# Kernel tuning notes

Measured on AMD Instinct MI355X. Metric: run time of the kernel, lower is better.

## Reference

```python
import jax, jax.numpy as jnp
import numpy as np

WH, WW = 8, 8
NUM_HEADS = 12
DIM = 384
N = WH * WW

def _rel_pos_index():
    # Swin relative position index, static [N, N] int array
    coords = np.stack(np.meshgrid(np.arange(WH), np.arange(WW), indexing='ij'))  # [2, wh, ww]
    cf = coords.reshape(2, -1)                      # [2, N]
    rel = cf[:, :, None] - cf[:, None, :]           # [2, N, N]
    rel = rel.transpose(1, 2, 0).copy()             # [N, N, 2]
    rel[..., 0] += WH - 1
    rel[..., 1] += WW - 1
    rel[..., 0] *= 2 * WW - 1
    return jnp.asarray(rel.sum(-1))                 # [N, N]

REL_IDX = _rel_pos_index()


def setup_inputs() -> dict:
    key = jax.random.key(0)
    ks = jax.random.split(key, 4)
    Bn = 4096
    x = jax.random.normal(ks[0], (Bn, N, DIM), dtype=jnp.float32)
    qkv_w = jax.random.normal(ks[1], (3 * DIM, DIM), dtype=jnp.float32) * 0.02
    qkv_b = jnp.zeros((3 * DIM,), dtype=jnp.float32)
    proj_w = jax.random.normal(ks[2], (DIM, DIM), dtype=jnp.float32) * 0.02
    proj_b = jnp.zeros((DIM,), dtype=jnp.float32)
    bias_table = jax.random.normal(ks[3], ((2 * WH - 1) * (2 * WW - 1), NUM_HEADS), dtype=jnp.float32) * 0.02
    return {"x": x, "qkv_w": qkv_w, "qkv_b": qkv_b, "proj_w": proj_w, "proj_b": proj_b, "bias_table": bias_table}


def reference(x, qkv_w, qkv_b, proj_w, proj_b, bias_table):
    Bn, n, C = x.shape
    H = NUM_HEADS
    hd = C // H
    scale = hd ** (-0.5)
    qkv = (x @ qkv_w.T + qkv_b).reshape(Bn, n, 3, H, hd)
    q = qkv[:, :, 0].transpose(0, 2, 1, 3)  # [Bn, H, n, hd]
    k = qkv[:, :, 1].transpose(0, 2, 1, 3)
    v = qkv[:, :, 2].transpose(0, 2, 1, 3)
    attn = jnp.einsum('bhqd,bhkd->bhqk', q, k) * scale  # [Bn, H, n, n]
    bias = bias_table[REL_IDX]                           # [n, n, H]
    attn = attn + bias.transpose(2, 0, 1)[None]          # add rel-pos bias
    attn = jax.nn.softmax(attn, axis=-1)
    out = jnp.einsum('bhqk,bhkd->bqhd', attn, v).reshape(Bn, n, C)
    return out @ proj_w.T + proj_b
```

## Files before the change

### kernel.cpp

```cpp
#include <hip/hip_runtime.h>

#define NT 64
#define NH 12
#define HD 32
#define DIM 384
#define NWIN 4096
#define TPB 512
#define PTPB 256

typedef __bf16 bf16;
typedef __bf16 bf16x8 __attribute__((ext_vector_type(8)));
typedef __bf16 bf16x4 __attribute__((ext_vector_type(4)));
typedef float floatx4 __attribute__((ext_vector_type(4)));

__device__ __align__(16) bf16 g_wqkv[3 * DIM * DIM];
__device__ __align__(16) bf16 g_wproj[DIM * DIM];
__device__ __align__(16) float g_biasT[NH * 225];

__global__ void convert_weights(const float* __restrict__ qkv_w,
                                const float* __restrict__ proj_w,
                                const float* __restrict__ bias_table) {
    int i = blockIdx.x * blockDim.x + threadIdx.x;
    if (i < 3 * DIM * DIM) g_wqkv[i] = (bf16)qkv_w[i];
    if (i < DIM * DIM)     g_wproj[i] = (bf16)proj_w[i];
    if (i < NH * 225) {
        int h = i / 225, ix = i % 225;
        g_biasT[i] = bias_table[ix * NH + h];
    }
}

__global__ __launch_bounds__(TPB, 4) void attn_kernel(
    const float* __restrict__ x,
    const float* __restrict__ qkv_b,
    float* __restrict__ out)
{
    __shared__ __align__(16) char smem[65288];
    bf16 (*sx)[392]      = (bf16(*)[392])smem;
    bf16 (*sq2)[64][40]  = (bf16(*)[64][40])smem;
    bf16 (*sk2)[64][40]  = (bf16(*)[64][40])(smem + 10240);
    bf16 (*svT2)[32][72] = (bf16(*)[32][72])(smem + 20480);
    float (*sp2)[64][66] = (float(*)[64][66])(smem + 29696);
    float (*sbias)[225]  = (float(*)[225])(smem + 63488);

    const int t    = threadIdx.x;
    const int win  = blockIdx.x;
    const int wave = t >> 6;
    const int lane = t & 63;
    const int quad = lane >> 4;
    const int l15  = lane & 15;

    {
        const float4* src = (const float4*)(x + (size_t)win * (NT * DIM));
        #pragma unroll
        for (int it = 0; it < (NT * DIM / 4) / TPB; ++it) {
            int i = t + it * TPB;
            float4 fv = src[i];
            int r = i / (DIM / 4);
            int c = (i % (DIM / 4)) * 4;
            bf16x4 bv;
            bv[0] = (bf16)fv.x; bv[1] = (bf16)fv.y;
            bv[2] = (bf16)fv.z; bv[3] = (bf16)fv.w;
            *(bf16x4*)&sx[r][c] = bv;
        }
    }
    __syncthreads();

    const int mt  = wave & 3;
    const int grp = wave >> 2;
    bf16x8 afrag[DIM / 32];
    #pragma unroll
    for (int ks = 0; ks < DIM / 32; ++ks)
        afrag[ks] = *(const bf16x8*)&sx[mt * 16 + l15][ks * 32 + quad * 8];
    __syncthreads();

    const float scale = 0.17677669529663687f;
    float* outw = out + (size_t)win * (NT * DIM);

    #pragma unroll 1
    for (int hp = 0; hp < NH / 2; ++hp) {
        if (t < 225)                      sbias[0][t]       = g_biasT[(hp * 2 + 0) * 225 + t];
        else if (t >= 256 && t < 481)     sbias[1][t - 256] = g_biasT[(hp * 2 + 1) * 225 + (t - 256)];

        #pragma unroll
        for (int jj = 0; jj < 6; ++jj) {
            const int hl  = jj / 3;
            const int j3  = jj % 3;
            const int nt  = grp * 3 + j3;
            const int s   = nt >> 1;
            const int nhh = (nt & 1) * 16;
            const int h   = hp * 2 + hl;
            const int wrow = s * DIM + h * HD + nhh + l15;
            const bf16* Wp = g_wqkv + (size_t)wrow * DIM + quad * 8;
            bf16x8 b[12];
            #pragma unroll
            for (int ks = 0; ks < 12; ++ks) b[ks] = *(const bf16x8*)(Wp + ks * 32);
            floatx4 acc = {0.f, 0.f, 0.f, 0.f};
            #pragma unroll
            for (int ks = 0; ks < 12; ++ks)
                acc = __builtin_amdgcn_mfma_f32_16x16x32_bf16(afrag[ks], b[ks], acc, 0, 0, 0);
            float bv = qkv_b[wrow];
            #pragma unroll
            for (int r = 0; r < 4; ++r) {
                int m = mt * 16 + quad * 4 + r;
                float v = acc[r] + bv;
                if (s == 0)      sq2[hl][m][nhh + l15] = (bf16)(v * scale);
                else if (s == 1) sk2[hl][m][nhh + l15] = (bf16)v;
                else             svT2[hl][nhh + l15][m] = (bf16)v;
            }
        }
        __syncthreads();

        #pragma unroll
        for (int jj = 0; jj < 4; ++jj) {
            int job = wave + jj * 8;
            int hl = job >> 4;
            int j4 = job & 15;
            int it = j4 & 3, jt = j4 >> 2;
            bf16x8 a = *(const bf16x8*)&sq2[hl][it * 16 + l15][quad * 8];
            bf16x8 b = *(const bf16x8*)&sk2[hl][jt * 16 + l15][quad * 8];
            floatx4 acc = {0.f, 0.f, 0.f, 0.f};
            acc = __builtin_amdgcn_mfma_f32_16x16x32_bf16(a, b, acc, 0, 0, 0);
            #pragma unroll
            for (int r = 0; r < 4; ++r) {
                int i = it * 16 + quad * 4 + r;
                int j = jt * 16 + l15;
                int yi = i >> 3, xi = i & 7, yj = j >> 3, xj = j & 7;
                int idx = (yi - yj + 7) * 15 + (xi - xj + 7);
                sp2[hl][i][j] = acc[r] + sbias[hl][idx];
            }
        }
        __syncthreads();

        {
            int r4 = t >> 2;
            int hl = r4 >> 6;
            int r  = r4 & 63;
            int o  = (t & 3) * 16;
            const float2* pr = (const float2*)&sp2[hl][r][0];
            float e[16];
            float mx = -1e30f;
            #pragma unroll
            for (int c = 0; c < 8; ++c) {
                float2 f2 = pr[(o >> 1) + c];
                e[2 * c] = f2.x; e[2 * c + 1] = f2.y;
                mx = fmaxf(mx, fmaxf(f2.x, f2.y));
            }
            mx = fmaxf(mx, __shfl_xor(mx, 1));
            mx = fmaxf(mx, __shfl_xor(mx, 2));
            float sum = 0.f;
            #pragma unroll
            for (int c = 0; c < 16; ++c) { e[c] = __expf(e[c] - mx); sum += e[c]; }
            sum += __shfl_xor(sum, 1);
            sum += __shfl_xor(sum, 2);
            float inv = 1.0f / sum;
            bf16* pw = (bf16*)&sp2[hl][r][0];
            #pragma unroll
            for (int k = 0; k < 4; ++k) {
                bf16x4 pv;
                #pragma unroll
                for (int z = 0; z < 4; ++z) pv[z] = (bf16)(e[4 * k + z] * inv);
                *(bf16x4*)&pw[o + 4 * k] = pv;
            }
        }
        __syncthreads();

        #pragma unroll
        for (int jj = 0; jj < 2; ++jj) {
            int job = wave + jj * 8;
            int hl = job >> 3;
            int j3 = job & 7;
            int pmt = j3 & 3, pnt = j3 >> 2;
            const bf16* prow = (const bf16*)&sp2[hl][pmt * 16 + l15][0];
            floatx4 acc = {0.f, 0.f, 0.f, 0.f};
            #pragma unroll
            for (int ks = 0; ks < 2; ++ks) {
                bf16x4 a0 = *(const bf16x4*)&prow[ks * 32 + quad * 8];
                bf16x4 a1 = *(const bf16x4*)&prow[ks * 32 + quad * 8 + 4];
                bf16x8 av;
                #pragma unroll
                for (int z = 0; z < 4; ++z) { av[z] = a0[z]; av[z + 4] = a1[z]; }
                bf16x8 b = *(const bf16x8*)&svT2[hl][pnt * 16 + l15][ks * 32 + quad * 8];
                acc = __builtin_amdgcn_mfma_f32_16x16x32_bf16(av, b, acc, 0, 0, 0);
            }
            int h = hp * 2 + hl;
            #pragma unroll
            for (int r = 0; r < 4; ++r) {
                int m = pmt * 16 + quad * 4 + r;
                outw[(size_t)m * DIM + h * HD + pnt * 16 + l15] = acc[r];
            }
        }
        __syncthreads();
    }
}

__global__ __launch_bounds__(PTPB, 3) void proj_kernel(
    const float* __restrict__ proj_b,
    float* __restrict__ out)
{
    __shared__ __align__(16) bf16 sa[NT][392];
    const int t    = threadIdx.x;
    const int wave = t >> 6;
    const int lane = t & 63;
    const int quad = lane >> 4;
    const int l15  = lane & 15;
    float* base = out + (size_t)blockIdx.x * (NT * DIM);

    {
        const float4* src = (const float4*)base;
        #pragma unroll
        for (int it = 0; it < (NT * DIM / 4) / PTPB; ++it) {
            int i = t + it * PTPB;
            float4 fv = src[i];
            int r = i / (DIM / 4);
            int c = (i % (DIM / 4)) * 4;
            bf16x4 bv;
            bv[0] = (bf16)fv.x; bv[1] = (bf16)fv.y;
            bv[2] = (bf16)fv.z; bv[3] = (bf16)fv.w;
            *(bf16x4*)&sa[r][c] = bv;
        }
    }
    __syncthreads();

    bf16x8 afrag[DIM / 32];
    #pragma unroll
    for (int ks = 0; ks < DIM / 32; ++ks)
        afrag[ks] = *(const bf16x8*)&sa[wave * 16 + l15][ks * 32 + quad * 8];

    #pragma unroll
    for (int nt = 0; nt < DIM / 16; ++nt) {
        const bf16* Wp = g_wproj + (size_t)(nt * 16 + l15) * DIM + quad * 8;
        bf16x8 b[12];
        #pragma unroll
        for (int ks = 0; ks < 12; ++ks) b[ks] = *(const bf16x8*)(Wp + ks * 32);
        floatx4 acc = {0.f, 0.f, 0.f, 0.f};
        #pragma unroll
        for (int ks = 0; ks < 12; ++ks)
            acc = __builtin_amdgcn_mfma_f32_16x16x32_bf16(afrag[ks], b[ks], acc, 0, 0, 0);
        float pb = proj_b[nt * 16 + l15];
        #pragma unroll
        for (int r = 0; r < 4; ++r)
            base[(size_t)(wave * 16 + quad * 4 + r) * DIM + nt * 16 + l15] = acc[r] + pb;
    }
}

extern "C" void kernel_launch(void* const* d_in, const int* in_sizes, int n_in,
                              void* d_out, int out_size, void* d_ws, size_t ws_size,
                              hipStream_t stream) {
    const float* x          = (const float*)d_in[0];
    const float* qkv_w      = (const float*)d_in[1];
    const float* qkv_b      = (const float*)d_in[2];
    const float* proj_w     = (const float*)d_in[3];
    const float* proj_b     = (const float*)d_in[4];
    const float* bias_table = (const float*)d_in[5];
    float* out = (float*)d_out;

    convert_weights<<<dim3((3 * DIM * DIM + 255) / 256), dim3(256), 0, stream>>>(qkv_w, proj_w, bias_table);
    attn_kernel<<<dim3(NWIN), dim3(TPB), 0, stream>>>(x, qkv_b, out);
    proj_kernel<<<dim3(NWIN), dim3(PTPB), 0, stream>>>(proj_b, out);
}
```

Baseline: 2.654 ms.

## Fuse scores, softmax and PV per wave in registers with double-buffered QKV

Each wave now computes the QK^T scores for its own 16 rows and one head, adds the relative-position bias, applies softmax with cross-lane shuffles in registers, and runs the PV matmul. This removes the fp32 score buffer in shared memory and three of the four block barriers per head pair. Q, K and V are double-buffered across head pairs, V^T and P use XOR-swizzled layouts, and the bias is precomputed into a full [H,64,64] table read from global memory. The x and attention-output staging through shared memory is replaced by direct per-lane float loads converted to bf16, and the GEMM accumulators are split into two chains. The costs are a larger shared-memory footprint, more global bias traffic, and uncoalesced direct global loads.

```diff
diff --git a/kernel.cpp b/kernel.cpp
--- a/kernel.cpp
+++ b/kernel.cpp
@@ -10,12 +10,11 @@
 
 typedef __bf16 bf16;
 typedef __bf16 bf16x8 __attribute__((ext_vector_type(8)));
-typedef __bf16 bf16x4 __attribute__((ext_vector_type(4)));
 typedef float floatx4 __attribute__((ext_vector_type(4)));
 
 __device__ __align__(16) bf16 g_wqkv[3 * DIM * DIM];
 __device__ __align__(16) bf16 g_wproj[DIM * DIM];
-__device__ __align__(16) float g_biasT[NH * 225];
+__device__ __align__(16) float g_biasF[NH * NT * NT];
 
 __global__ void convert_weights(const float* __restrict__ qkv_w,
                                 const float* __restrict__ proj_w,
@@ -23,10 +22,21 @@
     int i = blockIdx.x * blockDim.x + threadIdx.x;
     if (i < 3 * DIM * DIM) g_wqkv[i] = (bf16)qkv_w[i];
     if (i < DIM * DIM)     g_wproj[i] = (bf16)proj_w[i];
-    if (i < NH * 225) {
-        int h = i / 225, ix = i % 225;
-        g_biasT[i] = bias_table[ix * NH + h];
+    if (i < NH * NT * NT) {
+        int h = i >> 12, qk = i & 4095;
+        int q = qk >> 6, kv = qk & 63;
+        int idx = ((q >> 3) - (kv >> 3) + 7) * 15 + ((q & 7) - (kv & 7) + 7);
+        g_biasF[i] = bias_table[idx * NH + h];
     }
+}
+
+__device__ inline bf16x8 load_cvt8(const float* p) {
+    float4 f0 = *(const float4*)p;
+    float4 f1 = *(const float4*)(p + 4);
+    bf16x8 a;
+    a[0] = (bf16)f0.x; a[1] = (bf16)f0.y; a[2] = (bf16)f0.z; a[3] = (bf16)f0.w;
+    a[4] = (bf16)f1.x; a[5] = (bf16)f1.y; a[6] = (bf16)f1.z; a[7] = (bf16)f1.w;
+    return a;
 }
 
 __global__ __launch_bounds__(TPB, 4) void attn_kernel(
@@ -34,13 +44,11 @@
     const float* __restrict__ qkv_b,
     float* __restrict__ out)
 {
-    __shared__ __align__(16) char smem[65288];
-    bf16 (*sx)[392]      = (bf16(*)[392])smem;
-    bf16 (*sq2)[64][40]  = (bf16(*)[64][40])smem;
-    bf16 (*sk2)[64][40]  = (bf16(*)[64][40])(smem + 10240);
-    bf16 (*svT2)[32][72] = (bf16(*)[32][72])(smem + 20480);
-    float (*sp2)[64][66] = (float(*)[64][66])(smem + 29696);
-    float (*sbias)[225]  = (float(*)[225])(smem + 63488);
+    __shared__ __align__(16) char smem[73728];
+    bf16 (*sq)[2][64][40] = (bf16(*)[2][64][40])smem;
+    bf16 (*sk)[2][64][40] = (bf16(*)[2][64][40])(smem + 20480);
+    bf16* svT = (bf16*)(smem + 40960);
+    bf16* sP  = (bf16*)(smem + 57344);
 
     const int t    = threadIdx.x;
     const int win  = blockIdx.x;
@@ -48,156 +56,139 @@
     const int lane = t & 63;
     const int quad = lane >> 4;
     const int l15  = lane & 15;
-
-    {
-        const float4* src = (const float4*)(x + (size_t)win * (NT * DIM));
-        #pragma unroll
-        for (int it = 0; it < (NT * DIM / 4) / TPB; ++it) {
-            int i = t + it * TPB;
-            float4 fv = src[i];
-            int r = i / (DIM / 4);
-            int c = (i % (DIM / 4)) * 4;
-            bf16x4 bv;
-            bv[0] = (bf16)fv.x; bv[1] = (bf16)fv.y;
-            bv[2] = (bf16)fv.z; bv[3] = (bf16)fv.w;
-            *(bf16x4*)&sx[r][c] = bv;
-        }
-    }
-    __syncthreads();
-
-    const int mt  = wave & 3;
-    const int grp = wave >> 2;
-    bf16x8 afrag[DIM / 32];
+    const int mt   = wave & 3;
+    const int grp  = wave >> 2;
+
+    const float* xw = x + (size_t)win * (NT * DIM);
+    bf16x8 afrag[12];
     #pragma unroll
-    for (int ks = 0; ks < DIM / 32; ++ks)
-        afrag[ks] = *(const bf16x8*)&sx[mt * 16 + l15][ks * 32 + quad * 8];
-    __syncthreads();
+    for (int ks = 0; ks < 12; ++ks)
+        afrag[ks] = load_cvt8(xw + (mt * 16 + l15) * DIM + ks * 32 + quad * 8);
 
     const float scale = 0.17677669529663687f;
     float* outw = out + (size_t)win * (NT * DIM);
+    bf16* const sPw = sP + wave * 1024;
 
     #pragma unroll 1
     for (int hp = 0; hp < NH / 2; ++hp) {
-        if (t < 225)                      sbias[0][t]       = g_biasT[(hp * 2 + 0) * 225 + t];
-        else if (t >= 256 && t < 481)     sbias[1][t - 256] = g_biasT[(hp * 2 + 1) * 225 + (t - 256)];
+        const int buf = hp & 1;
 
         #pragma unroll
         for (int jj = 0; jj < 6; ++jj) {
             const int hl  = jj / 3;
-            const int j3  = jj % 3;
-            const int nt  = grp * 3 + j3;
+            const int nt  = grp * 3 + (jj % 3);
             const int s   = nt >> 1;
             const int nhh = (nt & 1) * 16;
             const int h   = hp * 2 + hl;
             const int wrow = s * DIM + h * HD + nhh + l15;
             const bf16* Wp = g_wqkv + (size_t)wrow * DIM + quad * 8;
-            bf16x8 b[12];
-            #pragma unroll
-            for (int ks = 0; ks < 12; ++ks) b[ks] = *(const bf16x8*)(Wp + ks * 32);
+            bf16x8 b0[6], b1[6];
+            #pragma unroll
+            for (int i = 0; i < 6; ++i) b0[i] = *(const bf16x8*)(Wp + i * 32);
+            #pragma unroll
+            for (int i = 0; i < 6; ++i) b1[i] = *(const bf16x8*)(Wp + 192 + i * 32);
+            floatx4 acc0 = {0.f, 0.f, 0.f, 0.f}, acc1 = {0.f, 0.f, 0.f, 0.f};
+            #pragma unroll
+            for (int i = 0; i < 6; ++i) {
+                acc0 = __builtin_amdgcn_mfma_f32_16x16x32_bf16(afrag[i],     b0[i], acc0, 0, 0, 0);
+                acc1 = __builtin_amdgcn_mfma_f32_16x16x32_bf16(afrag[6 + i], b1[i], acc1, 0, 0, 0);
+            }
+            const float bv = qkv_b[wrow];
+            #pragma unroll
+            for (int r = 0; r < 4; ++r) {
+                const int m = mt * 16 + quad * 4 + r;
+                const float v = acc0[r] + acc1[r] + bv;
+                if (s == 0)      sq[buf][hl][m][nhh + l15] = (bf16)(v * scale);
+                else if (s == 1) sk[buf][hl][m][nhh + l15] = (bf16)v;
+                else {
+                    const int row = nhh + l15;
+                    svT[(buf * 2 + hl) * 2048 + row * 64 + (m ^ ((row & 7) << 3))] = (bf16)v;
+                }
+            }
+        }
+        __syncthreads();
+
+        const int h = hp * 2 + grp;
+        const float* bias = g_biasF + h * (NT * NT) + (mt * 16 + quad * 4) * NT + l15;
+        float bb[4][4];
+        #pragma unroll
+        for (int jt = 0; jt < 4; ++jt)
+            #pragma unroll
+            for (int r = 0; r < 4; ++r)
+                bb[jt][r] = bias[r * NT + jt * 16];
+
+        const bf16x8 aq = *(const bf16x8*)&sq[buf][grp][mt * 16 + l15][quad * 8];
+        floatx4 sc[4];
+        #pragma unroll
+        for (int jt = 0; jt < 4; ++jt) {
+            const bf16x8 bk = *(const bf16x8*)&sk[buf][grp][jt * 16 + l15][quad * 8];
+            floatx4 z = {0.f, 0.f, 0.f, 0.f};
+            sc[jt] = __builtin_amdgcn_mfma_f32_16x16x32_bf16(aq, bk, z, 0, 0, 0);
+        }
+        #pragma unroll
+        for (int jt = 0; jt < 4; ++jt)
+            #pragma unroll
+            for (int r = 0; r < 4; ++r)
+                sc[jt][r] += bb[jt][r];
+
+        float mx[4], sm[4], inv[4];
+        #pragma unroll
+        for (int r = 0; r < 4; ++r) {
+            mx[r] = fmaxf(fmaxf(sc[0][r], sc[1][r]), fmaxf(sc[2][r], sc[3][r]));
+            mx[r] = fmaxf(mx[r], __shfl_xor(mx[r], 1));
+            mx[r] = fmaxf(mx[r], __shfl_xor(mx[r], 2));
+            mx[r] = fmaxf(mx[r], __shfl_xor(mx[r], 4));
+            mx[r] = fmaxf(mx[r], __shfl_xor(mx[r], 8));
+        }
+        float e[4][4];
+        #pragma unroll
+        for (int jt = 0; jt < 4; ++jt)
+            #pragma unroll
+            for (int r = 0; r < 4; ++r)
+                e[jt][r] = __expf(sc[jt][r] - mx[r]);
+        #pragma unroll
+        for (int r = 0; r < 4; ++r) {
+            sm[r] = (e[0][r] + e[1][r]) + (e[2][r] + e[3][r]);
+            sm[r] += __shfl_xor(sm[r], 1);
+            sm[r] += __shfl_xor(sm[r], 2);
+            sm[r] += __shfl_xor(sm[r], 4);
+            sm[r] += __shfl_xor(sm[r], 8);
+            inv[r] = 1.0f / sm[r];
+        }
+        #pragma unroll
+        for (int jt = 0; jt < 4; ++jt)
+            #pragma unroll
+            for (int r = 0; r < 4; ++r) {
+                const int row = quad * 4 + r;
+                const int col = jt * 16 + l15;
+                sPw[row * 64 + (col ^ ((row & 7) << 3))] = (bf16)(e[jt][r] * inv[r]);
+            }
+
+        bf16x8 ap[2];
+        #pragma unroll
+        for (int ks = 0; ks < 2; ++ks)
+            ap[ks] = *(const bf16x8*)&sPw[l15 * 64 + ((ks * 32 + quad * 8) ^ ((l15 & 7) << 3))];
+        const bf16* vb = svT + (buf * 2 + grp) * 2048;
+        #pragma unroll
+        for (int pnt = 0; pnt < 2; ++pnt) {
             floatx4 acc = {0.f, 0.f, 0.f, 0.f};
             #pragma unroll
-            for (int ks = 0; ks < 12; ++ks)
-                acc = __builtin_amdgcn_mfma_f32_16x16x32_bf16(afrag[ks], b[ks], acc, 0, 0, 0);
-            float bv = qkv_b[wrow];
-            #pragma unroll
-            for (int r = 0; r < 4; ++r) {
-                int m = mt * 16 + quad * 4 + r;
-                float v = acc[r] + bv;
-                if (s == 0)      sq2[hl][m][nhh + l15] = (bf16)(v * scale);
-                else if (s == 1) sk2[hl][m][nhh + l15] = (bf16)v;
-                else             svT2[hl][nhh + l15][m] = (bf16)v;
-            }
-        }
-        __syncthreads();
-
-        #pragma unroll
-        for (int jj = 0; jj < 4; ++jj) {
-            int job = wave + jj * 8;
-            int hl = job >> 4;
-            int j4 = job & 15;
-            int it = j4 & 3, jt = j4 >> 2;
-            bf16x8 a = *(const bf16x8*)&sq2[hl][it * 16 + l15][quad * 8];
-            bf16x8 b = *(const bf16x8*)&sk2[hl][jt * 16 + l15][quad * 8];
-            floatx4 acc = {0.f, 0.f, 0.f, 0.f};
-            acc = __builtin_amdgcn_mfma_f32_16x16x32_bf16(a, b, acc, 0, 0, 0);
-            #pragma unroll
-            for (int r = 0; r < 4; ++r) {
-                int i = it * 16 + quad * 4 + r;
-                int j = jt * 16 + l15;
-                int yi = i >> 3, xi = i & 7, yj = j >> 3, xj = j & 7;
-                int idx = (yi - yj + 7) * 15 + (xi - xj + 7);
-                sp2[hl][i][j] = acc[r] + sbias[hl][idx];
-            }
-        }
-        __syncthreads();
-
-        {
-            int r4 = t >> 2;
-            int hl = r4 >> 6;
-            int r  = r4 & 63;
-            int o  = (t & 3) * 16;
-            const float2* pr = (const float2*)&sp2[hl][r][0];
-            float e[16];
-            float mx = -1e30f;
-            #pragma unroll
-            for (int c = 0; c < 8; ++c) {
-                float2 f2 = pr[(o >> 1) + c];
-                e[2 * c] = f2.x; e[2 * c + 1] = f2.y;
-                mx = fmaxf(mx, fmaxf(f2.x, f2.y));
-            }
-            mx = fmaxf(mx, __shfl_xor(mx, 1));
-            mx = fmaxf(mx, __shfl_xor(mx, 2));
-            float sum = 0.f;
-            #pragma unroll
-            for (int c = 0; c < 16; ++c) { e[c] = __expf(e[c] - mx); sum += e[c]; }
-            sum += __shfl_xor(sum, 1);
-            sum += __shfl_xor(sum, 2);
-            float inv = 1.0f / sum;
-            bf16* pw = (bf16*)&sp2[hl][r][0];
-            #pragma unroll
-            for (int k = 0; k < 4; ++k) {
-                bf16x4 pv;
-                #pragma unroll
-                for (int z = 0; z < 4; ++z) pv[z] = (bf16)(e[4 * k + z] * inv);
-                *(bf16x4*)&pw[o + 4 * k] = pv;
-            }
-        }
-        __syncthreads();
-
-        #pragma unroll
-        for (int jj = 0; jj < 2; ++jj) {
-            int job = wave + jj * 8;
-            int hl = job >> 3;
-            int j3 = job & 7;
-            int pmt = j3 & 3, pnt = j3 >> 2;
-            const bf16* prow = (const bf16*)&sp2[hl][pmt * 16 + l15][0];
-            floatx4 acc = {0.f, 0.f, 0.f, 0.f};
-            #pragma unroll
             for (int ks = 0; ks < 2; ++ks) {
-                bf16x4 a0 = *(const bf16x4*)&prow[ks * 32 + quad * 8];
-                bf16x4 a1 = *(const bf16x4*)&prow[ks * 32 + quad * 8 + 4];
-                bf16x8 av;
-                #pragma unroll
-                for (int z = 0; z < 4; ++z) { av[z] = a0[z]; av[z + 4] = a1[z]; }
-                bf16x8 b = *(const bf16x8*)&svT2[hl][pnt * 16 + l15][ks * 32 + quad * 8];
-                acc = __builtin_amdgcn_mfma_f32_16x16x32_bf16(av, b, acc, 0, 0, 0);
-            }
-            int h = hp * 2 + hl;
-            #pragma unroll
-            for (int r = 0; r < 4; ++r) {
-                int m = pmt * 16 + quad * 4 + r;
-                outw[(size_t)m * DIM + h * HD + pnt * 16 + l15] = acc[r];
-            }
-        }
-        __syncthreads();
+                const int vrow = pnt * 16 + l15;
+                const bf16x8 bv = *(const bf16x8*)&vb[vrow * 64 + ((ks * 32 + quad * 8) ^ ((vrow & 7) << 3))];
+                acc = __builtin_amdgcn_mfma_f32_16x16x32_bf16(ap[ks], bv, acc, 0, 0, 0);
+            }
+            #pragma unroll
+            for (int r = 0; r < 4; ++r)
+                outw[(size_t)(mt * 16 + quad * 4 + r) * DIM + h * HD + pnt * 16 + l15] = acc[r];
+        }
     }
 }
 
-__global__ __launch_bounds__(PTPB, 3) void proj_kernel(
+__global__ __launch_bounds__(PTPB, 4) void proj_kernel(
     const float* __restrict__ proj_b,
     float* __restrict__ out)
 {
-    __shared__ __align__(16) bf16 sa[NT][392];
     const int t    = threadIdx.x;
     const int wave = t >> 6;
     const int lane = t & 63;
@@ -205,41 +196,29 @@
     const int l15  = lane & 15;
     float* base = out + (size_t)blockIdx.x * (NT * DIM);
 
-    {
-        const float4* src = (const float4*)base;
-        #pragma unroll
-        for (int it = 0; it < (NT * DIM / 4) / PTPB; ++it) {
-            int i = t + it * PTPB;
-            float4 fv = src[i];
-            int r = i / (DIM / 4);
-            int c = (i % (DIM / 4)) * 4;
-            bf16x4 bv;
-            bv[0] = (bf16)fv.x; bv[1] = (bf16)fv.y;
-            bv[2] = (bf16)fv.z; bv[3] = (bf16)fv.w;
-            *(bf16x4*)&sa[r][c] = bv;
-        }
-    }
-    __syncthreads();
-
-    bf16x8 afrag[DIM / 32];
+    bf16x8 afrag[12];
     #pragma unroll
-    for (int ks = 0; ks < DIM / 32; ++ks)
-        afrag[ks] = *(const bf16x8*)&sa[wave * 16 + l15][ks * 32 + quad * 8];
+    for (int ks = 0; ks < 12; ++ks)
+        afrag[ks] = load_cvt8(base + (wave * 16 + l15) * DIM + ks * 32 + quad * 8);
 
     #pragma unroll
     for (int nt = 0; nt < DIM / 16; ++nt) {
         const bf16* Wp = g_wproj + (size_t)(nt * 16 + l15) * DIM + quad * 8;
-        bf16x8 b[12];
-        #pragma unroll
-        for (int ks = 0; ks < 12; ++ks) b[ks] = *(const bf16x8*)(Wp + ks * 32);
-        floatx4 acc = {0.f, 0.f, 0.f, 0.f};
-        #pragma unroll
-        for (int ks = 0; ks < 12; ++ks)
-            acc = __builtin_amdgcn_mfma_f32_16x16x32_bf16(afrag[ks], b[ks], acc, 0, 0, 0);
-        float pb = proj_b[nt * 16 + l15];
+        bf16x8 b0[6], b1[6];
+        #pragma unroll
+        for (int i = 0; i < 6; ++i) b0[i] = *(const bf16x8*)(Wp + i * 32);
+        #pragma unroll
+        for (int i = 0; i < 6; ++i) b1[i] = *(const bf16x8*)(Wp + 192 + i * 32);
+        floatx4 acc0 = {0.f, 0.f, 0.f, 0.f}, acc1 = {0.f, 0.f, 0.f, 0.f};
+        #pragma unroll
+        for (int i = 0; i < 6; ++i) {
+            acc0 = __builtin_amdgcn_mfma_f32_16x16x32_bf16(afrag[i],     b0[i], acc0, 0, 0, 0);
+            acc1 = __builtin_amdgcn_mfma_f32_16x16x32_bf16(afrag[6 + i], b1[i], acc1, 0, 0, 0);
+        }
+        const float pb = proj_b[nt * 16 + l15];
         #pragma unroll
         for (int r = 0; r < 4; ++r)
-            base[(size_t)(wave * 16 + quad * 4 + r) * DIM + nt * 16 + l15] = acc[r] + pb;
+            base[(size_t)(wave * 16 + quad * 4 + r) * DIM + nt * 16 + l15] = acc0[r] + acc1[r] + pb;
     }
 }
 
```

Result: slower. 2.763 ms (+4.1%).
